# Performance work log

Measured on AMD Instinct MI355X. Metric: run time of the kernel, lower is better.

The kernel has to match this reference:

```python
import jax, jax.numpy as jnp
import numpy as np

B, H, S, D = 4, 16, 2048, 64

def setup_inputs() -> dict:
    key = jax.random.key(0)
    kq, kk, kv = jax.random.split(key, 3)
    Q = jax.random.normal(kq, (B, H, S, D), dtype=jnp.float32)
    K = jax.random.normal(kk, (B, H, S, D), dtype=jnp.float32)
    V = jax.random.normal(kv, (B, H, S, D), dtype=jnp.float32)
    return {"Q": Q, "K": K, "V": V}

def reference(Q, K, V):
    d = Q.shape[-1]
    scale = jnp.sqrt(jnp.asarray(d, dtype=Q.dtype))
    # scores: [B, H, S, S]
    scores = jnp.einsum('bhqd,bhkd->bhqk', Q, K) / scale
    attn = jax.nn.softmax(scores, axis=-1)
    out = jnp.einsum('bhqk,bhkd->bhqd', attn, V)  # [B,H,S,D]
    # permute to [B,S,H,D] then merge heads -> [B,S,H*D]
    b, h, s, dd = out.shape
    return out.transpose(0, 2, 1, 3).reshape(b, s, h * dd)
```

## Files before the change

### kernel.cpp

```cpp
#include <hip/hip_runtime.h>
#include <hip/hip_bf16.h>


#define B_ 4
#define H_ 16
#define S_ 2048
#define D_ 64
#define BH 64
#define NKT 32
#define TILE_USH 4096
#define ARR_USH ((size_t)BH * NKT * TILE_USH)
#define WS_NEED (2 * ARR_USH * 2)
#define QSCALE 0.18033688011112042f

typedef float  f4 __attribute__((ext_vector_type(4)));
typedef short  s4 __attribute__((ext_vector_type(4)));
typedef short  s8 __attribute__((ext_vector_type(8)));
typedef unsigned short ushort_t;

__device__ __forceinline__ unsigned short f2bf(float x) {
  unsigned int u = __float_as_uint(x);
  u += 0x7fffu + ((u >> 16) & 1u);
  return (unsigned short)(u >> 16);
}
__device__ __forceinline__ unsigned int pk_bf16(float a, float b) {
  __hip_bfloat162 h = __float22bfloat162_rn(make_float2(a, b));
  union { __hip_bfloat162 h2; unsigned int u; } cv; cv.h2 = h; return cv.u;
}
__device__ __forceinline__ void splitbf_rne(float x, unsigned short& hi, unsigned short& lo) {
  hi = f2bf(x);
  float hf = __uint_as_float((unsigned int)hi << 16);
  lo = f2bf(x - hf);
}
__device__ __forceinline__ void splitbf(float x, unsigned short& hi, unsigned short& lo) {
  unsigned int u = __float_as_uint(x);
  hi = (unsigned short)(u >> 16);
  float hf = __uint_as_float(u & 0xffff0000u);
  lo = (unsigned short)(__float_as_uint(x - hf) >> 16);
}

typedef __attribute__((address_space(1))) const unsigned int* gas_t;
typedef __attribute__((address_space(3))) unsigned int* las_t;
__device__ __forceinline__ void gl_lds16(const void* g, void* l) {
  __builtin_amdgcn_global_load_lds((gas_t)g, (las_t)l, 16, 0, 0);
}

__global__ __launch_bounds__(256)
void prep(const float* __restrict__ K, const float* __restrict__ V,
          ushort_t* __restrict__ KH, ushort_t* __restrict__ VT) {
  __shared__ float Vf[64][68];
  const int tile = blockIdx.x;
  const int t = threadIdx.x;

  const float* vsrc = V + (size_t)tile * 4096;
  float4 vv[4];
  int srow[4], dcol[4];
  #pragma unroll
  for (int r = 0; r < 4; ++r) {
    int f = r * 256 + t; srow[r] = f >> 4; dcol[r] = (f & 15) << 2;
    vv[r] = *(const float4*)(vsrc + srow[r] * 64 + dcol[r]);
  }
  {
    const float* src0 = K + (size_t)tile * 4096;
    #pragma unroll
    for (int u = 0; u < 2; ++u) {
      unsigned int i = u * 256 + t;
      unsigned int row = i >> 3, c = (i & 7) ^ (row & 7);
      const float* src = src0 + row * 64 + c * 8;
      float4 a = *(const float4*)src;
      float4 b = *(const float4*)(src + 4);
      unsigned int d0 = pk_bf16(a.x, a.y), d1 = pk_bf16(a.z, a.w);
      unsigned int d2 = pk_bf16(b.x, b.y), d3 = pk_bf16(b.z, b.w);
      uint4 out = make_uint4(d0, d1, d2, d3);
      *(uint4*)(KH + (size_t)tile * TILE_USH + i * 8) = out;
    }
  }
  #pragma unroll
  for (int r = 0; r < 4; ++r) {
    int pcol = dcol[r] ^ (((srow[r] >> 3) & 3) << 2);
    *(float4*)&Vf[srow[r]][pcol] = vv[r];
  }
  __syncthreads();
  #pragma unroll
  for (int u = 0; u < 2; ++u) {
    unsigned int i = u * 256 + t;
    unsigned int drow = i >> 3, c = (i & 7) ^ (drow & 7);
    const unsigned int col = drow ^ ((c & 3) << 2);
    unsigned int d0 = pk_bf16(Vf[c * 8 + 0][col], Vf[c * 8 + 1][col]);
    unsigned int d1 = pk_bf16(Vf[c * 8 + 2][col], Vf[c * 8 + 3][col]);
    unsigned int d2 = pk_bf16(Vf[c * 8 + 4][col], Vf[c * 8 + 5][col]);
    unsigned int d3 = pk_bf16(Vf[c * 8 + 6][col], Vf[c * 8 + 7][col]);
    uint4 out = make_uint4(d0, d1, d2, d3);
    *(uint4*)(VT + (size_t)tile * TILE_USH + i * 8) = out;
  }
}

__global__ __launch_bounds__(256, 4)
void attn9(const float* __restrict__ Q, const ushort_t* __restrict__ KH,
           const ushort_t* __restrict__ VT, float* __restrict__ O) {
  __shared__ ushort_t KhS[2][TILE_USH];
  __shared__ ushort_t VtS[2][TILE_USH];

  const int t    = threadIdx.x;
  const int w    = t >> 6;
  const int lane = t & 63;
  const int g    = lane >> 4;
  const int ln   = lane & 15;

  const unsigned int n = blockIdx.x;
  const int bh = (int)((n >> 7) * 8 + (n & 7));
  const int q0 = (int)(((n >> 3) & 15) * 128);

  const size_t tb = (size_t)bh * NKT * TILE_USH;
  const unsigned int cb = w * 128;

  #pragma unroll
  for (int j = 0; j < 2; ++j) {
    const unsigned int ch = cb + 64u * j;
    const size_t go = tb + (size_t)(ch + lane) * 8;
    gl_lds16(KH + go, &KhS[0][ch * 8]);
    gl_lds16(VT + go, &VtS[0][ch * 8]);
  }

  s8 qfh[2][2], qfl[2][2];
  #pragma unroll
  for (int sub = 0; sub < 2; ++sub) {
    const int q = q0 + 32 * w + 16 * sub + ln;
    #pragma unroll
    for (int ks = 0; ks < 2; ++ks) {
      const float* qp = Q + ((size_t)bh * S_ + q) * 64 + 32 * ks + 8 * g;
      float4 a = *(const float4*)qp;
      float4 b = *(const float4*)(qp + 4);
      float xs[8] = {a.x, a.y, a.z, a.w, b.x, b.y, b.z, b.w};
      s8 hv, lv;
      #pragma unroll
      for (int j = 0; j < 8; ++j) {
        unsigned short h, lo; splitbf_rne(xs[j] * QSCALE, h, lo);
        hv[j] = (short)h; lv[j] = (short)lo;
      }
      qfh[sub][ks] = hv; qfl[sub][ks] = lv;
    }
  }

  f4 oacc[2][4];
  f4 lacc[2];
  #pragma unroll
  for (int s = 0; s < 2; ++s) {
    lacc[s] = (f4)0.0f;
    #pragma unroll
    for (int d = 0; d < 4; ++d) oacc[s][d] = (f4)0.0f;
  }

  s8 ones;
  #pragma unroll
  for (int j = 0; j < 8; ++j) ones[j] = (short)0x3F80;

  unsigned int foff[2];
  #pragma unroll
  for (int ks = 0; ks < 2; ++ks)
    foff[ks] = (unsigned)ln * 128u + (unsigned)(((4 * ks + g) ^ (ln & 7)) * 16);

  const bool glt2 = (g < 2);
  const bool sr   = (g == 0) || (g == 3);

  for (int kt = 0; kt < NKT; ++kt) {
    const int cur = kt & 1;
    __syncthreads();

    if (kt + 1 < NKT) {
      const size_t tbase = tb + (size_t)(kt + 1) * TILE_USH;
      const int nb = cur ^ 1;
      #pragma unroll
      for (int j = 0; j < 2; ++j) {
        const unsigned int ch = cb + 64u * j;
        const size_t go = tbase + (size_t)(ch + lane) * 8;
        gl_lds16(KH + go, &KhS[nb][ch * 8]);
        gl_lds16(VT + go, &VtS[nb][ch * 8]);
      }
    }

    const char* khb = (const char*)&KhS[cur][0];
    const char* vtb = (const char*)&VtS[cur][0];

    #pragma unroll
    for (int h = 0; h < 2; ++h) {
      s8 k00 = *(const s8*)(khb + (2 * h + 0) * 2048 + foff[0]);
      s8 k01 = *(const s8*)(khb + (2 * h + 0) * 2048 + foff[1]);
      s8 k10 = *(const s8*)(khb + (2 * h + 1) * 2048 + foff[0]);
      s8 k11 = *(const s8*)(khb + (2 * h + 1) * 2048 + foff[1]);

      s8 pa[2];
      #pragma unroll
      for (int sub = 0; sub < 2; ++sub) {
        f4 s0 = (f4)0.0f, s1 = (f4)0.0f;
        s0 = __builtin_amdgcn_mfma_f32_16x16x32_bf16(k00, qfh[sub][0], s0, 0, 0, 0);
        s0 = __builtin_amdgcn_mfma_f32_16x16x32_bf16(k00, qfl[sub][0], s0, 0, 0, 0);
        s0 = __builtin_amdgcn_mfma_f32_16x16x32_bf16(k01, qfh[sub][1], s0, 0, 0, 0);
        s0 = __builtin_amdgcn_mfma_f32_16x16x32_bf16(k01, qfl[sub][1], s0, 0, 0, 0);
        s1 = __builtin_amdgcn_mfma_f32_16x16x32_bf16(k10, qfh[sub][0], s1, 0, 0, 0);
        s1 = __builtin_amdgcn_mfma_f32_16x16x32_bf16(k10, qfl[sub][0], s1, 0, 0, 0);
        s1 = __builtin_amdgcn_mfma_f32_16x16x32_bf16(k11, qfh[sub][1], s1, 0, 0, 0);
        s1 = __builtin_amdgcn_mfma_f32_16x16x32_bf16(k11, qfl[sub][1], s1, 0, 0, 0);

        unsigned int a0 = pk_bf16(__builtin_amdgcn_exp2f(s0[0]),
                                  __builtin_amdgcn_exp2f(s0[1]));
        unsigned int a1 = pk_bf16(__builtin_amdgcn_exp2f(s0[2]),
                                  __builtin_amdgcn_exp2f(s0[3]));
        unsigned int b0 = pk_bf16(__builtin_amdgcn_exp2f(s1[0]),
                                  __builtin_amdgcn_exp2f(s1[1]));
        unsigned int b1 = pk_bf16(__builtin_amdgcn_exp2f(s1[2]),
                                  __builtin_amdgcn_exp2f(s1[3]));

        unsigned int t0 = glt2 ? b0 : a0, t1 = glt2 ? b1 : a1;
        unsigned int r0 = (unsigned int)__shfl_xor((int)t0, 32);
        unsigned int r1 = (unsigned int)__shfl_xor((int)t1, 32);
        unsigned int own0 = (g == 1) ? a0 : b0, own1 = (g == 1) ? a1 : b1;
        unsigned int u0 = sr ? r0 : own0, u1 = sr ? r1 : own1;
        unsigned int q0v = (unsigned int)__shfl_xor((int)u0, 16);
        unsigned int q1v = (unsigned int)__shfl_xor((int)u1, 16);
        union { unsigned int u[4]; s8 v; } cvp;
        cvp.u[0] = (g == 0) ? a0 : (g == 2) ? r0 : q0v;
        cvp.u[1] = (g == 0) ? a1 : (g == 2) ? r1 : q1v;
        cvp.u[2] = (g == 3) ? b0 : (g == 1) ? r0 : q0v;
        cvp.u[3] = (g == 3) ? b1 : (g == 1) ? r1 : q1v;
        pa[sub] = cvp.v;
        lacc[sub] = __builtin_amdgcn_mfma_f32_16x16x32_bf16(pa[sub], ones, lacc[sub], 0, 0, 0);
      }

      #pragma unroll
      for (int dt = 0; dt < 4; ++dt) {
        s8 vb = *(const s8*)(vtb + dt * 2048 + foff[h]);
        #pragma unroll
        for (int sub = 0; sub < 2; ++sub)
          oacc[sub][dt] = __builtin_amdgcn_mfma_f32_16x16x32_bf16(pa[sub], vb, oacc[sub][dt], 0, 0, 0);
      }
    }
  }

  const int b = bh >> 4, hh = bh & 15;
  #pragma unroll
  for (int sub = 0; sub < 2; ++sub)
    #pragma unroll
    for (int r = 0; r < 4; ++r) {
      const float inv = 1.0f / lacc[sub][r];
      const int q = q0 + 32 * w + 16 * sub + 4 * g + r;
      float* dst = O + ((size_t)b * S_ + q) * (H_ * D_) + hh * 64;
      #pragma unroll
      for (int dt = 0; dt < 4; ++dt)
        dst[16 * dt + ln] = oacc[sub][dt][r] * inv;
    }
}

#define KQ_STR 72
#define VP_STR 76
__global__ __launch_bounds__(256, 2)
void attn_mfma(const float* __restrict__ Q, const float* __restrict__ K,
               const float* __restrict__ V, float* __restrict__ O) {
  __shared__ __align__(16) unsigned short Qh[64][KQ_STR];
  __shared__ __align__(16) unsigned short Ql[64][KQ_STR];
  __shared__ __align__(16) unsigned short Kh[64][KQ_STR];
  __shared__ __align__(16) unsigned short Kl[64][KQ_STR];
  __shared__ __align__(16) unsigned short Vt[64][VP_STR];
  __shared__ __align__(16) unsigned short Pb2[4][16][VP_STR];
  const int t = threadIdx.x, w = t >> 6, lane = t & 63, g = lane >> 4, ln = lane & 15;
  const int bh = blockIdx.x, q0 = blockIdx.y * 64;
  const size_t base = (size_t)bh * S_ * D_;
  {
    const float* Qg = Q + base + (size_t)q0 * D_;
    #pragma unroll
    for (int r = 0; r < 4; ++r) {
      int f = r * 256 + t, row = f >> 4, c4 = (f & 15) << 2;
      float4 v = *(const float4*)(Qg + row * 64 + c4);
      s4 hv, lv; unsigned short hb, lb;
      splitbf(v.x * 0.125f, hb, lb); hv[0] = (short)hb; lv[0] = (short)lb;
      splitbf(v.y * 0.125f, hb, lb); hv[1] = (short)hb; lv[1] = (short)lb;
      splitbf(v.z * 0.125f, hb, lb); hv[2] = (short)hb; lv[2] = (short)lb;
      splitbf(v.w * 0.125f, hb, lb); hv[3] = (short)hb; lv[3] = (short)lb;
      *(s4*)&Qh[row][c4] = hv; *(s4*)&Ql[row][c4] = lv;
    }
  }
  __syncthreads();
  s8 qfh[2], qfl[2];
  #pragma unroll
  for (int ks = 0; ks < 2; ++ks) {
    qfh[ks] = *(const s8*)&Qh[16 * w + ln][ks * 32 + 8 * g];
    qfl[ks] = *(const s8*)&Ql[16 * w + ln][ks * 32 + 8 * g];
  }
  f4 oacc[4]; float m[4], l[4];
  #pragma unroll
  for (int i = 0; i < 4; ++i) { oacc[i] = (f4)0.0f; m[i] = -1e30f; l[i] = 0.0f; }
  const float* Kg = K + base; const float* Vg = V + base;
  float4 kreg[4], vreg[4];
  #pragma unroll
  for (int r = 0; r < 4; ++r) {
    int f = r * 256 + t, row = f >> 4, c4 = (f & 15) << 2;
    kreg[r] = *(const float4*)(Kg + row * 64 + c4);
  }
  #pragma unroll
  for (int j = 0; j < 2; ++j) {
    int it = j * 256 + t, kp = it >> 4, c4 = (it & 15) << 2;
    vreg[2 * j] = *(const float4*)(Vg + (2 * kp) * 64 + c4);
    vreg[2 * j + 1] = *(const float4*)(Vg + (2 * kp + 1) * 64 + c4);
  }
  for (int kt = 0; kt < S_ / 64; ++kt) {
    __syncthreads();
    #pragma unroll
    for (int r = 0; r < 4; ++r) {
      int f = r * 256 + t, row = f >> 4, c4 = (f & 15) << 2;
      float4 v = kreg[r];
      s4 hv, lv; unsigned short hb, lb;
      splitbf(v.x, hb, lb); hv[0] = (short)hb; lv[0] = (short)lb;
      splitbf(v.y, hb, lb); hv[1] = (short)hb; lv[1] = (short)lb;
      splitbf(v.z, hb, lb); hv[2] = (short)hb; lv[2] = (short)lb;
      splitbf(v.w, hb, lb); hv[3] = (short)hb; lv[3] = (short)lb;
      *(s4*)&Kh[row][c4] = hv; *(s4*)&Kl[row][c4] = lv;
    }
    #pragma unroll
    for (int j = 0; j < 2; ++j) {
      int it = j * 256 + t, kp = it >> 4, c4 = (it & 15) << 2;
      float4 a = vreg[2 * j], b = vreg[2 * j + 1];
      float xa[4] = {a.x, a.y, a.z, a.w}, xb[4] = {b.x, b.y, b.z, b.w};
      #pragma unroll
      for (int i = 0; i < 4; ++i) {
        unsigned int pk = (unsigned int)f2bf(xa[i]) | ((unsigned int)f2bf(xb[i]) << 16);
        *(unsigned int*)&Vt[c4 + i][2 * kp] = pk;
      }
    }
    if (kt + 1 < S_ / 64) {
      const float* Kt = Kg + (size_t)(kt + 1) * 4096;
      const float* Vn = Vg + (size_t)(kt + 1) * 4096;
      #pragma unroll
      for (int r = 0; r < 4; ++r) {
        int f = r * 256 + t, row = f >> 4, c4 = (f & 15) << 2;
        kreg[r] = *(const float4*)(Kt + row * 64 + c4);
      }
      #pragma unroll
      for (int j = 0; j < 2; ++j) {
        int it = j * 256 + t, kp = it >> 4, c4 = (it & 15) << 2;
        vreg[2 * j] = *(const float4*)(Vn + (2 * kp) * 64 + c4);
        vreg[2 * j + 1] = *(const float4*)(Vn + (2 * kp + 1) * 64 + c4);
      }
    }
    __syncthreads();
    f4 sacc[4];
    #pragma unroll
    for (int nt = 0; nt < 4; ++nt) sacc[nt] = (f4)0.0f;
    #pragma unroll
    for (int nt = 0; nt < 4; ++nt)
      #pragma unroll
      for (int ks = 0; ks < 2; ++ks) {
        s8 kh = *(const s8*)&Kh[16 * nt + ln][ks * 32 + 8 * g];
        s8 kl = *(const s8*)&Kl[16 * nt + ln][ks * 32 + 8 * g];
        sacc[nt] = __builtin_amdgcn_mfma_f32_16x16x32_bf16(qfh[ks], kh, sacc[nt], 0, 0, 0);
        sacc[nt] = __builtin_amdgcn_mfma_f32_16x16x32_bf16(qfl[ks], kh, sacc[nt], 0, 0, 0);
        sacc[nt] = __builtin_amdgcn_mfma_f32_16x16x32_bf16(qfh[ks], kl, sacc[nt], 0, 0, 0);
      }
    #pragma unroll
    for (int r = 0; r < 4; ++r) {
      float rm = fmaxf(fmaxf(sacc[0][r], sacc[1][r]), fmaxf(sacc[2][r], sacc[3][r]));
      rm = fmaxf(rm, __shfl_xor(rm, 1)); rm = fmaxf(rm, __shfl_xor(rm, 2));
      rm = fmaxf(rm, __shfl_xor(rm, 4)); rm = fmaxf(rm, __shfl_xor(rm, 8));
      float mn = fmaxf(m[r], rm);
      float alpha = __expf(m[r] - mn); m[r] = mn;
      float p0 = __expf(sacc[0][r] - mn), p1 = __expf(sacc[1][r] - mn);
      float p2 = __expf(sacc[2][r] - mn), p3 = __expf(sacc[3][r] - mn);
      float rs = p0 + p1 + p2 + p3;
      rs += __shfl_xor(rs, 1); rs += __shfl_xor(rs, 2);
      rs += __shfl_xor(rs, 4); rs += __shfl_xor(rs, 8);
      l[r] = l[r] * alpha + rs;
      oacc[0][r] *= alpha; oacc[1][r] *= alpha; oacc[2][r] *= alpha; oacc[3][r] *= alpha;
      const int row = 4 * g + r;
      Pb2[w][row][ln] = f2bf(p0); Pb2[w][row][ln + 16] = f2bf(p1);
      Pb2[w][row][ln + 32] = f2bf(p2); Pb2[w][row][ln + 48] = f2bf(p3);
    }
    #pragma unroll
    for (int ks = 0; ks < 2; ++ks) {
      s4 pa0 = *(const s4*)&Pb2[w][ln][ks * 32 + 8 * g];
      s4 pa1 = *(const s4*)&Pb2[w][ln][ks * 32 + 8 * g + 4];
      s8 pa = __builtin_shufflevector(pa0, pa1, 0, 1, 2, 3, 4, 5, 6, 7);
      #pragma unroll
      for (int dt = 0; dt < 4; ++dt) {
        s4 vb0 = *(const s4*)&Vt[16 * dt + ln][ks * 32 + 8 * g];
        s4 vb1 = *(const s4*)&Vt[16 * dt + ln][ks * 32 + 8 * g + 4];
        s8 vb = __builtin_shufflevector(vb0, vb1, 0, 1, 2, 3, 4, 5, 6, 7);
        oacc[dt] = __builtin_amdgcn_mfma_f32_16x16x32_bf16(pa, vb, oacc[dt], 0, 0, 0);
      }
    }
  }
  const int b = bh >> 4, h = bh & 15;
  #pragma unroll
  for (int r = 0; r < 4; ++r) {
    const int q = q0 + 16 * w + 4 * g + r;
    const float inv = 1.0f / l[r];
    float* dst = O + ((size_t)b * S_ + q) * (H_ * D_) + h * 64;
    #pragma unroll
    for (int dt = 0; dt < 4; ++dt) dst[16 * dt + ln] = oacc[dt][r] * inv;
  }
}

extern "C" void kernel_launch(void* const* d_in, const int* in_sizes, int n_in,
                              void* d_out, int out_size, void* d_ws, size_t ws_size,
                              hipStream_t stream) {
  const float* Q = (const float*)d_in[0];
  const float* K = (const float*)d_in[1];
  const float* V = (const float*)d_in[2];
  float* Out = (float*)d_out;
  if (ws_size >= WS_NEED) {
    ushort_t* KHp = (ushort_t*)d_ws;
    ushort_t* VTp = KHp + ARR_USH;
    hipLaunchKernelGGL(prep, dim3(2048), dim3(256), 0, stream, K, V, KHp, VTp);
    hipLaunchKernelGGL(attn9, dim3(1024), dim3(256), 0, stream, Q, KHp, VTp, Out);
  } else {
    hipLaunchKernelGGL(attn_mfma, dim3(BH, S_ / 64), dim3(256), 0, stream, Q, K, V, Out);
  }
}
```

Baseline: 231.2 us.

## Permute V-transpose key order in prep to remove lane shuffles in attention

```diff
diff --git a/kernel.cpp b/kernel.cpp
--- a/kernel.cpp
+++ b/kernel.cpp
@@ -85,19 +85,21 @@
   for (int u = 0; u < 2; ++u) {
     unsigned int i = u * 256 + t;
     unsigned int drow = i >> 3, c = (i & 7) ^ (drow & 7);
-    const unsigned int col = drow ^ ((c & 3) << 2);
-    unsigned int d0 = pk_bf16(Vf[c * 8 + 0][col], Vf[c * 8 + 1][col]);
-    unsigned int d1 = pk_bf16(Vf[c * 8 + 2][col], Vf[c * 8 + 3][col]);
-    unsigned int d2 = pk_bf16(Vf[c * 8 + 4][col], Vf[c * 8 + 5][col]);
-    unsigned int d3 = pk_bf16(Vf[c * 8 + 6][col], Vf[c * 8 + 7][col]);
+    const unsigned int ka   = ((c >> 2) << 5) + ((c & 3) << 2);
+    const unsigned int colA = drow ^ ((c & 2) << 1);
+    const unsigned int colB = colA ^ 8;
+    unsigned int d0 = pk_bf16(Vf[ka +  0][colA], Vf[ka +  1][colA]);
+    unsigned int d1 = pk_bf16(Vf[ka +  2][colA], Vf[ka +  3][colA]);
+    unsigned int d2 = pk_bf16(Vf[ka + 16][colB], Vf[ka + 17][colB]);
+    unsigned int d3 = pk_bf16(Vf[ka + 18][colB], Vf[ka + 19][colB]);
     uint4 out = make_uint4(d0, d1, d2, d3);
     *(uint4*)(VT + (size_t)tile * TILE_USH + i * 8) = out;
   }
 }
 
 __global__ __launch_bounds__(256, 4)
-void attn9(const float* __restrict__ Q, const ushort_t* __restrict__ KH,
-           const ushort_t* __restrict__ VT, float* __restrict__ O) {
+void attn10(const float* __restrict__ Q, const ushort_t* __restrict__ KH,
+            const ushort_t* __restrict__ VT, float* __restrict__ O) {
   __shared__ ushort_t KhS[2][TILE_USH];
   __shared__ ushort_t VtS[2][TILE_USH];
 
@@ -159,9 +161,6 @@
   #pragma unroll
   for (int ks = 0; ks < 2; ++ks)
     foff[ks] = (unsigned)ln * 128u + (unsigned)(((4 * ks + g) ^ (ln & 7)) * 16);
-
-  const bool glt2 = (g < 2);
-  const bool sr   = (g == 0) || (g == 3);
 
   for (int kt = 0; kt < NKT; ++kt) {
     const int cur = kt & 1;
@@ -210,19 +209,8 @@
                                   __builtin_amdgcn_exp2f(s1[1]));
         unsigned int b1 = pk_bf16(__builtin_amdgcn_exp2f(s1[2]),
                                   __builtin_amdgcn_exp2f(s1[3]));
-
-        unsigned int t0 = glt2 ? b0 : a0, t1 = glt2 ? b1 : a1;
-        unsigned int r0 = (unsigned int)__shfl_xor((int)t0, 32);
-        unsigned int r1 = (unsigned int)__shfl_xor((int)t1, 32);
-        unsigned int own0 = (g == 1) ? a0 : b0, own1 = (g == 1) ? a1 : b1;
-        unsigned int u0 = sr ? r0 : own0, u1 = sr ? r1 : own1;
-        unsigned int q0v = (unsigned int)__shfl_xor((int)u0, 16);
-        unsigned int q1v = (unsigned int)__shfl_xor((int)u1, 16);
         union { unsigned int u[4]; s8 v; } cvp;
-        cvp.u[0] = (g == 0) ? a0 : (g == 2) ? r0 : q0v;
-        cvp.u[1] = (g == 0) ? a1 : (g == 2) ? r1 : q1v;
-        cvp.u[2] = (g == 3) ? b0 : (g == 1) ? r0 : q0v;
-        cvp.u[3] = (g == 3) ? b1 : (g == 1) ? r1 : q1v;
+        cvp.u[0] = a0; cvp.u[1] = a1; cvp.u[2] = b0; cvp.u[3] = b1;
         pa[sub] = cvp.v;
         lacc[sub] = __builtin_amdgcn_mfma_f32_16x16x32_bf16(pa[sub], ones, lacc[sub], 0, 0, 0);
       }
@@ -409,7 +397,7 @@
     ushort_t* KHp = (ushort_t*)d_ws;
     ushort_t* VTp = KHp + ARR_USH;
     hipLaunchKernelGGL(prep, dim3(2048), dim3(256), 0, stream, K, V, KHp, VTp);
-    hipLaunchKernelGGL(attn9, dim3(1024), dim3(256), 0, stream, Q, KHp, VTp, Out);
+    hipLaunchKernelGGL(attn10, dim3(1024), dim3(256), 0, stream, Q, KHp, VTp, Out);
   } else {
     hipLaunchKernelGGL(attn_mfma, dim3(BH, S_ / 64), dim3(256), 0, stream, Q, K, V, Out);
   }
```

Result: faster. 214.2 us (-7.3%).
